# Optimization experiments

Hardware: AMD Instinct MI355X
Metric: run time of the kernel (lower is better)

Reference implementation:

```python
import jax, jax.numpy as jnp
import numpy as np

ID, IH, IW = 8, 16, 16
HEADS, DIM_HEAD = 8, 32
INP, OUP = 256, 256
B = 4
N = ID * IH * IW  # 2048
INNER = HEADS * DIM_HEAD  # 256
SCALE = DIM_HEAD ** -0.5


def _make_relative_pos():
    # Faithful to the torch ctor: 3D coords, pairwise diffs, linearize, shift to >=0
    z, y, x = np.meshgrid(np.arange(ID), np.arange(IH), np.arange(IW), indexing='ij')
    coords = np.stack([z.ravel(), y.ravel(), x.ravel()], axis=1)  # [N,3]
    rel = coords[:, None, :] - coords[None, :, :]                 # [N,N,3]
    rp = rel[:, :, 0] * (IH * IW) + rel[:, :, 1] * IW + rel[:, :, 2]
    rp = rp - rp.min()
    return jnp.asarray(rp, dtype=jnp.int32)                       # [N,N]


def setup_inputs() -> dict:
    key = jax.random.key(0)
    k1, k2, k3, k4, k5 = jax.random.split(key, 5)
    table_size = ID * IH * IW * 8  # 16384, as in nn.Embedding ctor
    return {
        "x": jax.random.normal(k1, (B, N, INP), dtype=jnp.float32),
        "w_qkv": jax.random.normal(k2, (INP, 3 * INNER), dtype=jnp.float32) * (INP ** -0.5),
        "bias_table": jax.random.normal(k3, (table_size, 1), dtype=jnp.float32),
        "w_out": jax.random.normal(k4, (INNER, OUP), dtype=jnp.float32) * (INNER ** -0.5),
        "b_out": jax.random.normal(k5, (OUP,), dtype=jnp.float32),
        "relative_pos": _make_relative_pos(),
    }


def reference(x, w_qkv, bias_table, w_out, b_out, relative_pos):
    Bb, Nn, C = x.shape
    qkv = x @ w_qkv                                   # [B, N, 3*H*D]
    qkv = qkv.reshape(Bb, Nn, 3, HEADS, DIM_HEAD)
    qkv = jnp.transpose(qkv, (2, 0, 3, 1, 4))         # [3, B, H, N, D]
    q, k, v = qkv[0], qkv[1], qkv[2]
    q = q * SCALE
    attn = jnp.einsum('bhnd,bhmd->bhnm', q, k)        # [B, H, N, N]
    bias = bias_table[relative_pos, 0]                # [N, N], shared across B,H
    attn = attn + bias
    attn = jax.nn.softmax(attn, axis=-1)
    out = jnp.einsum('bhnm,bhmd->bhnd', attn, v)      # [B, H, N, D]
    out = jnp.transpose(out, (0, 2, 1, 3)).reshape(Bb, Nn, INNER)
    return out @ w_out + b_out                        # dropout p=0 -> identity
```

## Files before the change

### kernel.cpp

```cpp
#include <hip/hip_runtime.h>

typedef unsigned short u16;
typedef unsigned int u32;
typedef __attribute__((ext_vector_type(8))) short bf16x8;
typedef __attribute__((ext_vector_type(4))) float f32x4;

#define MFMA16(a, b, c) __builtin_amdgcn_mfma_f32_16x16x32_bf16(a, b, c, 0, 0, 0)

__device__ __forceinline__ float hw_exp2(float x) { return __builtin_amdgcn_exp2f(x); }

__device__ __forceinline__ u16 f2bf(float f) {
    union { float f; u32 i; } v; v.f = f;
    u32 x = v.i;
    return (u16)((x + 0x7FFFu + ((x >> 16) & 1u)) >> 16);
}

__global__ __launch_bounds__(256) void k_prep(const float* __restrict__ x,
                                              const float* __restrict__ wqkv,
                                              const float* __restrict__ wout,
                                              u16* __restrict__ xb,
                                              u16* __restrict__ wqkvT,
                                              u16* __restrict__ woutT) {
    const float QSCALE2 = 0.2550566756538019f;
    int bx = blockIdx.x, tid = threadIdx.x;
    if (bx < 1024) {
        int base = bx * 2048 + tid * 8;
        float4 a = *(const float4*)(x + base);
        float4 b = *(const float4*)(x + base + 4);
        uint4 r;
        r.x = f2bf(a.x) | ((u32)f2bf(a.y) << 16);
        r.y = f2bf(a.z) | ((u32)f2bf(a.w) << 16);
        r.z = f2bf(b.x) | ((u32)f2bf(b.y) << 16);
        r.w = f2bf(b.z) | ((u32)f2bf(b.w) << 16);
        *(uint4*)(xb + base) = r;
    } else if (bx < 1792) {
        int idx = (bx - 1024) * 256 + tid;
        int n = idx >> 8, kk = idx & 255;
        float sc = (n < 256) ? QSCALE2 : 1.0f;
        wqkvT[idx] = f2bf(wqkv[kk * 768 + n] * sc);
    } else {
        int idx = (bx - 1792) * 256 + tid;
        int n = idx >> 8, kk = idx & 255;
        woutT[idx] = f2bf(wout[kk * 256 + n]);
    }
}

__global__ __launch_bounds__(256) void k_gemm_qkv(const u16* __restrict__ xb,
                                                  const u16* __restrict__ wT,
                                                  u16* __restrict__ qkv) {
    const int tid = threadIdx.x;
    const int wave = tid >> 6, lane = tid & 63, quad = lane >> 4, ql = lane & 15;
    const int mbase = blockIdx.x * 128 + (wave & 1) * 64;
    const int nbase = blockIdx.y * 64 + (wave >> 1) * 32;
    f32x4 acc[4][2];
#pragma unroll
    for (int i = 0; i < 4; ++i)
#pragma unroll
        for (int j = 0; j < 2; ++j) acc[i][j] = (f32x4){0.f, 0.f, 0.f, 0.f};
#pragma unroll
    for (int ks = 0; ks < 8; ++ks) {
        bf16x8 af[4], bfm[2];
#pragma unroll
        for (int ms = 0; ms < 4; ++ms)
            af[ms] = *(const bf16x8*)(xb + (size_t)(mbase + ms * 16 + ql) * 256 + ks * 32 + quad * 8);
#pragma unroll
        for (int ns = 0; ns < 2; ++ns)
            bfm[ns] = *(const bf16x8*)(wT + (size_t)(nbase + ns * 16 + ql) * 256 + ks * 32 + quad * 8);
#pragma unroll
        for (int ms = 0; ms < 4; ++ms)
#pragma unroll
            for (int ns = 0; ns < 2; ++ns)
                acc[ms][ns] = MFMA16(af[ms], bfm[ns], acc[ms][ns]);
    }
#pragma unroll
    for (int ms = 0; ms < 4; ++ms)
#pragma unroll
        for (int ns = 0; ns < 2; ++ns) {
            int colb = nbase + ns * 16;
            int t = colb >> 8;
            int Mrow0 = mbase + ms * 16 + quad * 4;
            int bb = Mrow0 >> 11, nn0 = Mrow0 & 2047;
            int col = colb + ql;
            int h = (col & 255) >> 5, d = col & 31;
            if (t == 2) {
                u16 e0 = f2bf(acc[ms][ns][0]), e1 = f2bf(acc[ms][ns][1]);
                u16 e2 = f2bf(acc[ms][ns][2]), e3 = f2bf(acc[ms][ns][3]);
                uint2 pp; pp.x = e0 | ((u32)e1 << 16); pp.y = e2 | ((u32)e3 << 16);
                *(uint2*)(qkv + (size_t)2 * 2097152 + (size_t)(bb * 8 + h) * 65536 +
                          (size_t)d * 2048 + nn0) = pp;
            } else {
#pragma unroll
                for (int r = 0; r < 4; ++r)
                    qkv[(size_t)t * 2097152 + ((size_t)(bb * 8 + h) * 2048 + nn0 + r) * 32 + d] =
                        f2bf(acc[ms][ns][r]);
            }
        }
}

__global__ __launch_bounds__(256, 3) void k_attn(const u16* __restrict__ q,
                                                 const u16* __restrict__ k,
                                                 const u16* __restrict__ vT,
                                                 const float* __restrict__ table,
                                                 u16* __restrict__ att) {
    __shared__ __align__(16) u16 kbuf[2][2][2048];
    __shared__ __align__(16) u16 vbuf[2][2][2048];
    __shared__ float tbl2[2112];
    __shared__ u32 pT[4][16 * 36];
    const int tid = threadIdx.x;
    const int bh = blockIdx.x & 31, qt = blockIdx.x >> 5;
    const int wave = tid >> 6, lane = tid & 63, quad = lane >> 4, ql = lane & 15;
    const float LOG2E = 1.4426950408889634f;

    const u16* kbh = k + (size_t)bh * 65536;
    const u16* vbh = vT + (size_t)bh * 65536;

    const int krow = wave * 16 + (lane >> 2);
    const u16* kg = kbh + krow * 32 + ((((lane & 3) ^ ((lane >> 3) & 3))) << 3);
    const int vd = wave * 8 + (lane >> 3);
    const u16* vg = vbh + (size_t)vd * 2048 + (((lane & 7) ^ (vd & 7)) << 3);

#define GLDS(SRC, DST) __builtin_amdgcn_global_load_lds(                         \
        (const __attribute__((address_space(1))) void*)(SRC),                    \
        (__attribute__((address_space(3))) void*)(DST), 16, 0, 0)
#define DMA(BUF, PAIR) do {                                                      \
    GLDS(kg + (PAIR) * 4096,        &kbuf[BUF][0][wave * 512]);                  \
    GLDS(kg + (PAIR) * 4096 + 2048, &kbuf[BUF][1][wave * 512]);                  \
    GLDS(vg + (PAIR) * 128,         &vbuf[BUF][0][wave * 512]);                  \
    GLDS(vg + (PAIR) * 128 + 64,    &vbuf[BUF][1][wave * 512]);                  \
} while (0)

    DMA(0, 0);

    const float4* tg = (const float4*)(table + qt * 64);
    for (int i = tid; i < 528; i += 256) {
        float4 t = tg[i];
        t.x *= LOG2E; t.y *= LOG2E; t.z *= LOG2E; t.w *= LOG2E;
        ((float4*)tbl2)[i] = t;
    }

    const int qr0 = qt * 64 + wave * 16 + ql;
    const bf16x8 qf = *(const bf16x8*)(q + ((size_t)bh * 2048 + qr0) * 32 + quad * 8);
    const int bloc = wave * 16 + ql + 2047 - quad * 4;
    const int kro = ((quad ^ ((ql >> 1) & 3)) << 3);
    const int pbase = ql * 36;

    bf16x8 ones;
#pragma unroll
    for (int i = 0; i < 8; ++i) ones[i] = (short)0x3F80;

    f32x4 oT0 = {0.f, 0.f, 0.f, 0.f}, oT1 = {0.f, 0.f, 0.f, 0.f}, oL = {0.f, 0.f, 0.f, 0.f};
    u32* pw = &pT[wave][0];

    __syncthreads();

    for (int pr = 0; pr < 16; ++pr) {
        const int buf = pr & 1;
        if (pr < 15) DMA(buf ^ 1, pr + 1);

#pragma unroll
        for (int t = 0; t < 2; ++t) {
            const int kt = pr * 2 + t;
            const u16* kb = &kbuf[buf][t][0];
            const u16* vb = &vbuf[buf][t][0];
            bf16x8 kf[4], vf[4];
#pragma unroll
            for (int j = 0; j < 4; ++j)
                kf[j] = *(const bf16x8*)(kb + (j * 16 + ql) * 32 + kro);
#pragma unroll
            for (int f = 0; f < 4; ++f) {
                int c = f >> 1, dt = f & 1;
                vf[f] = *(const bf16x8*)(vb + (dt * 16 + ql) * 64 +
                                         (((c * 4 + quad) ^ (ql & 7)) << 3));
            }

            f32x4 z = {0.f, 0.f, 0.f, 0.f};
            f32x4 s[4];
#pragma unroll
            for (int j = 0; j < 4; ++j) s[j] = MFMA16(kf[j], qf, z);
#pragma unroll
            for (int j = 0; j < 4; ++j)
#pragma unroll
                for (int r = 0; r < 4; ++r)
                    s[j][r] = hw_exp2(s[j][r] + tbl2[bloc - kt * 64 - j * 16 - r]);
#pragma unroll
            for (int j = 0; j < 4; ++j) {
                uint2 w;
                w.x = __builtin_amdgcn_perm(__float_as_uint(s[j][1]),
                                            __float_as_uint(s[j][0]), 0x07060302u);
                w.y = __builtin_amdgcn_perm(__float_as_uint(s[j][3]),
                                            __float_as_uint(s[j][2]), 0x07060302u);
                *(uint2*)&pw[pbase + j * 8 + quad * 2] = w;
            }
#pragma unroll
            for (int c = 0; c < 2; ++c) {
                bf16x8 pa = *(const bf16x8*)&pw[pbase + c * 16 + quad * 4];
                oT0 = MFMA16(vf[c * 2 + 0], pa, oT0);
                oT1 = MFMA16(vf[c * 2 + 1], pa, oT1);
                oL  = MFMA16(ones, pa, oL);
            }
        }
        __syncthreads();
    }
#undef DMA
#undef GLDS

    float inv = 1.0f / oL[0];
    size_t base = ((size_t)bh * 2048 + qr0) * 32;
#pragma unroll
    for (int dt = 0; dt < 2; ++dt) {
        u16 e0 = f2bf(oT0[0] * inv), e1 = f2bf(oT0[1] * inv);
        u16 e2 = f2bf(oT0[2] * inv), e3 = f2bf(oT0[3] * inv);
        if (dt == 1) {
            e0 = f2bf(oT1[0] * inv); e1 = f2bf(oT1[1] * inv);
            e2 = f2bf(oT1[2] * inv); e3 = f2bf(oT1[3] * inv);
        }
        uint2 pp; pp.x = e0 | ((u32)e1 << 16); pp.y = e2 | ((u32)e3 << 16);
        *(uint2*)(att + base + dt * 16 + quad * 4) = pp;
    }
}

__global__ __launch_bounds__(256) void k_gemm_out(const u16* __restrict__ attq,
                                                  const u16* __restrict__ wT,
                                                  const float* __restrict__ bout,
                                                  float* __restrict__ out) {
    const int tid = threadIdx.x;
    const int wave = tid >> 6, lane = tid & 63, quad = lane >> 4, ql = lane & 15;
    const int mbase = blockIdx.x * 128 + (wave & 1) * 64;
    const int nbase = blockIdx.y * 64 + (wave >> 1) * 32;
    f32x4 acc[4][2];
#pragma unroll
    for (int i = 0; i < 4; ++i)
#pragma unroll
        for (int j = 0; j < 2; ++j) acc[i][j] = (f32x4){0.f, 0.f, 0.f, 0.f};
#pragma unroll
    for (int ks = 0; ks < 8; ++ks) {
        bf16x8 af[4], bfm[2];
#pragma unroll
        for (int ms = 0; ms < 4; ++ms) {
            int row = mbase + ms * 16 + ql;
            af[ms] = *(const bf16x8*)(attq +
                ((size_t)((row >> 11) * 8 + ks) * 2048 + (row & 2047)) * 32 + quad * 8);
        }
#pragma unroll
        for (int ns = 0; ns < 2; ++ns)
            bfm[ns] = *(const bf16x8*)(wT + (size_t)(nbase + ns * 16 + ql) * 256 + ks * 32 + quad * 8);
#pragma unroll
        for (int ms = 0; ms < 4; ++ms)
#pragma unroll
            for (int ns = 0; ns < 2; ++ns)
                acc[ms][ns] = MFMA16(af[ms], bfm[ns], acc[ms][ns]);
    }
#pragma unroll
    for (int ms = 0; ms < 4; ++ms)
#pragma unroll
        for (int ns = 0; ns < 2; ++ns)
#pragma unroll
            for (int r = 0; r < 4; ++r) {
                int Mrow = mbase + ms * 16 + quad * 4 + r;
                int col = nbase + ns * 16 + ql;
                out[(size_t)Mrow * 256 + col] = acc[ms][ns][r] + bout[col];
            }
}

extern "C" void kernel_launch(void* const* d_in, const int* in_sizes, int n_in,
                              void* d_out, int out_size, void* d_ws, size_t ws_size,
                              hipStream_t stream) {
    const float* x    = (const float*)d_in[0];
    const float* wqkv = (const float*)d_in[1];
    const float* btab = (const float*)d_in[2];
    const float* wout = (const float*)d_in[3];
    const float* bout = (const float*)d_in[4];
    float* out = (float*)d_out;

    if (ws_size < (size_t)13107200) return;
    u16* ws = (u16*)d_ws;
    u16* wqkvT = ws;
    u16* woutT = wqkvT + 196608;
    u16* qkv   = woutT + 65536;
    u16* xb    = (u16*)d_out;

    hipLaunchKernelGGL(k_prep, dim3(2048), dim3(256), 0, stream, x, wqkv, wout, xb, wqkvT, woutT);
    hipLaunchKernelGGL(k_gemm_qkv, dim3(64, 12), dim3(256), 0, stream, xb, wqkvT, qkv);
    hipLaunchKernelGGL(k_attn, dim3(1024), dim3(256), 0, stream,
                       qkv, qkv + 2097152, qkv + 2 * 2097152, btab, qkv);
    hipLaunchKernelGGL(k_gemm_out, dim3(64, 4), dim3(256), 0, stream, qkv, woutT, bout, out);
}
```

Baseline: 147.9 us.

## Process two query sub-tiles per wave to reuse K/V tiles in attention

Each wave now handles 32 query rows (two 16-row sub-tiles) instead of 16, so every K/V tile loaded into shared memory and into registers serves twice as many queries. The grid is halved to 512 blocks and the bias table slice and P scratch buffers grow accordingly. The aim is to cut redundant K/V global traffic and LDS reads per unit of work. The cost is higher register and LDS use per block, fewer blocks to fill the GPU, and a change of the occupancy hint to 4.

Result: no change. 146.8 us (-0.7%).

```diff
diff --git a/kernel.cpp b/kernel.cpp
--- a/kernel.cpp
+++ b/kernel.cpp
@@ -97,15 +97,15 @@
         }
 }
 
-__global__ __launch_bounds__(256, 3) void k_attn(const u16* __restrict__ q,
+__global__ __launch_bounds__(256, 4) void k_attn(const u16* __restrict__ q,
                                                  const u16* __restrict__ k,
                                                  const u16* __restrict__ vT,
                                                  const float* __restrict__ table,
                                                  u16* __restrict__ att) {
     __shared__ __align__(16) u16 kbuf[2][2][2048];
     __shared__ __align__(16) u16 vbuf[2][2][2048];
-    __shared__ float tbl2[2112];
-    __shared__ u32 pT[4][16 * 36];
+    __shared__ float tbl2[2176];
+    __shared__ u32 pT[8][16 * 36];
     const int tid = threadIdx.x;
     const int bh = blockIdx.x & 31, qt = blockIdx.x >> 5;
     const int wave = tid >> 6, lane = tid & 63, quad = lane >> 4, ql = lane & 15;
@@ -131,16 +131,18 @@
 
     DMA(0, 0);
 
-    const float4* tg = (const float4*)(table + qt * 64);
-    for (int i = tid; i < 528; i += 256) {
+    const float4* tg = (const float4*)(table + qt * 128);
+    for (int i = tid; i < 544; i += 256) {
         float4 t = tg[i];
         t.x *= LOG2E; t.y *= LOG2E; t.z *= LOG2E; t.w *= LOG2E;
         ((float4*)tbl2)[i] = t;
     }
 
-    const int qr0 = qt * 64 + wave * 16 + ql;
-    const bf16x8 qf = *(const bf16x8*)(q + ((size_t)bh * 2048 + qr0) * 32 + quad * 8);
-    const int bloc = wave * 16 + ql + 2047 - quad * 4;
+    const int qr0 = qt * 128 + wave * 32 + ql;
+    bf16x8 qf[2];
+    qf[0] = *(const bf16x8*)(q + ((size_t)bh * 2048 + qr0) * 32 + quad * 8);
+    qf[1] = *(const bf16x8*)(q + ((size_t)bh * 2048 + qr0 + 16) * 32 + quad * 8);
+    const int bloc0 = wave * 32 + ql + 2047 - quad * 4;
     const int kro = ((quad ^ ((ql >> 1) & 3)) << 3);
     const int pbase = ql * 36;
 
@@ -148,8 +150,13 @@
 #pragma unroll
     for (int i = 0; i < 8; ++i) ones[i] = (short)0x3F80;
 
-    f32x4 oT0 = {0.f, 0.f, 0.f, 0.f}, oT1 = {0.f, 0.f, 0.f, 0.f}, oL = {0.f, 0.f, 0.f, 0.f};
-    u32* pw = &pT[wave][0];
+    f32x4 oT0[2], oT1[2], oL[2];
+#pragma unroll
+    for (int qh = 0; qh < 2; ++qh) {
+        oT0[qh] = (f32x4){0.f, 0.f, 0.f, 0.f};
+        oT1[qh] = (f32x4){0.f, 0.f, 0.f, 0.f};
+        oL[qh]  = (f32x4){0.f, 0.f, 0.f, 0.f};
+    }
 
     __syncthreads();
 
@@ -173,30 +180,36 @@
                                          (((c * 4 + quad) ^ (ql & 7)) << 3));
             }
 
-            f32x4 z = {0.f, 0.f, 0.f, 0.f};
-            f32x4 s[4];
-#pragma unroll
-            for (int j = 0; j < 4; ++j) s[j] = MFMA16(kf[j], qf, z);
-#pragma unroll
-            for (int j = 0; j < 4; ++j)
-#pragma unroll
-                for (int r = 0; r < 4; ++r)
-                    s[j][r] = hw_exp2(s[j][r] + tbl2[bloc - kt * 64 - j * 16 - r]);
-#pragma unroll
-            for (int j = 0; j < 4; ++j) {
-                uint2 w;
-                w.x = __builtin_amdgcn_perm(__float_as_uint(s[j][1]),
-                                            __float_as_uint(s[j][0]), 0x07060302u);
-                w.y = __builtin_amdgcn_perm(__float_as_uint(s[j][3]),
-                                            __float_as_uint(s[j][2]), 0x07060302u);
-                *(uint2*)&pw[pbase + j * 8 + quad * 2] = w;
-            }
-#pragma unroll
-            for (int c = 0; c < 2; ++c) {
-                bf16x8 pa = *(const bf16x8*)&pw[pbase + c * 16 + quad * 4];
-                oT0 = MFMA16(vf[c * 2 + 0], pa, oT0);
-                oT1 = MFMA16(vf[c * 2 + 1], pa, oT1);
-                oL  = MFMA16(ones, pa, oL);
+#pragma unroll
+            for (int qh = 0; qh < 2; ++qh) {
+                f32x4 z = {0.f, 0.f, 0.f, 0.f};
+                f32x4 s[4];
+#pragma unroll
+                for (int j = 0; j < 4; ++j) s[j] = MFMA16(kf[j], qf[qh], z);
+#pragma unroll
+                for (int j = 0; j < 4; ++j) {
+                    const float* tb = &tbl2[bloc0 + qh * 16 - kt * 64 - j * 16 - 3];
+#pragma unroll
+                    for (int r = 0; r < 4; ++r)
+                        s[j][r] = hw_exp2(s[j][r] + tb[3 - r]);
+                }
+                u32* pw = &pT[wave * 2 + qh][0];
+#pragma unroll
+                for (int j = 0; j < 4; ++j) {
+                    uint2 w;
+                    w.x = __builtin_amdgcn_perm(__float_as_uint(s[j][1]),
+                                                __float_as_uint(s[j][0]), 0x07060302u);
+                    w.y = __builtin_amdgcn_perm(__float_as_uint(s[j][3]),
+                                                __float_as_uint(s[j][2]), 0x07060302u);
+                    *(uint2*)&pw[pbase + j * 8 + quad * 2] = w;
+                }
+#pragma unroll
+                for (int c = 0; c < 2; ++c) {
+                    bf16x8 pa = *(const bf16x8*)&pw[pbase + c * 16 + quad * 4];
+                    oT0[qh] = MFMA16(vf[c * 2 + 0], pa, oT0[qh]);
+                    oT1[qh] = MFMA16(vf[c * 2 + 1], pa, oT1[qh]);
+                    oL[qh]  = MFMA16(ones, pa, oL[qh]);
+                }
             }
         }
         __syncthreads();
@@ -204,18 +217,18 @@
 #undef DMA
 #undef GLDS
 
-    float inv = 1.0f / oL[0];
-    size_t base = ((size_t)bh * 2048 + qr0) * 32;
-#pragma unroll
-    for (int dt = 0; dt < 2; ++dt) {
-        u16 e0 = f2bf(oT0[0] * inv), e1 = f2bf(oT0[1] * inv);
-        u16 e2 = f2bf(oT0[2] * inv), e3 = f2bf(oT0[3] * inv);
-        if (dt == 1) {
-            e0 = f2bf(oT1[0] * inv); e1 = f2bf(oT1[1] * inv);
-            e2 = f2bf(oT1[2] * inv); e3 = f2bf(oT1[3] * inv);
+#pragma unroll
+    for (int qh = 0; qh < 2; ++qh) {
+        float inv = 1.0f / oL[qh][0];
+        size_t base = ((size_t)bh * 2048 + qr0 + qh * 16) * 32;
+#pragma unroll
+        for (int dt = 0; dt < 2; ++dt) {
+            const f32x4& o = dt ? oT1[qh] : oT0[qh];
+            u16 e0 = f2bf(o[0] * inv), e1 = f2bf(o[1] * inv);
+            u16 e2 = f2bf(o[2] * inv), e3 = f2bf(o[3] * inv);
+            uint2 pp; pp.x = e0 | ((u32)e1 << 16); pp.y = e2 | ((u32)e3 << 16);
+            *(uint2*)(att + base + dt * 16 + quad * 4) = pp;
         }
-        uint2 pp; pp.x = e0 | ((u32)e1 << 16); pp.y = e2 | ((u32)e3 << 16);
-        *(uint2*)(att + base + dt * 16 + quad * 4) = pp;
     }
 }
 
@@ -281,7 +294,7 @@
 
     hipLaunchKernelGGL(k_prep, dim3(2048), dim3(256), 0, stream, x, wqkv, wout, xb, wqkvT, woutT);
     hipLaunchKernelGGL(k_gemm_qkv, dim3(64, 12), dim3(256), 0, stream, xb, wqkvT, qkv);
-    hipLaunchKernelGGL(k_attn, dim3(1024), dim3(256), 0, stream,
+    hipLaunchKernelGGL(k_attn, dim3(512), dim3(256), 0, stream,
                        qkv, qkv + 2097152, qkv + 2 * 2097152, btab, qkv);
     hipLaunchKernelGGL(k_gemm_out, dim3(64, 4), dim3(256), 0, stream, qkv, woutT, bout, out);
 }
```
